# Optimization experiments

Hardware: AMD Instinct MI355X
Metric: run time of the kernel (lower is better)

The kernel has to match this reference:

```python
import jax, jax.numpy as jnp
import numpy as np

HD = 64          # head_dim
PX = 32          # patches_x
PY = 32          # patches_y
IW = 512.0       # image_width
IH = 512.0       # image_height
C = 4            # cameras
B = 1
H = 12
S = C * PX * PY  # 4096


def _rope_coeffs(pos, feat_dim):
    nf = feat_dim // 2
    freqs = 100.0 ** (-jnp.arange(nf, dtype=jnp.float32) / nf)  # freq_base=100, freq_scale=1
    ang = pos[:, None].astype(jnp.float32) * freqs[None, :]
    # broadcast shape (1, seqlen, 1, nf)
    return jnp.cos(ang)[None, :, None, :], jnp.sin(ang)[None, :, None, :]


def _rope(x, cs, inverse=False):
    cos, sin = cs
    h = x.shape[-1] // 2
    xi, yi = x[..., :h], x[..., h:]
    if inverse:
        return jnp.concatenate([cos * xi - sin * yi, sin * xi + cos * yi], -1)
    return jnp.concatenate([cos * xi + sin * yi, -sin * xi + cos * yi], -1)


def _proj(x, M):
    # x: (b, s, n, f), M: (b, c, D, D) per-camera projection applied to D-sized sub-blocks
    b, s, n, f = x.shape
    c, D = M.shape[1], M.shape[-1]
    xr = x.reshape(b, c, s // c, n, f // D, D)
    return jnp.einsum('bcij,bcpnkj->bcpnki', M, xr).reshape(b, s, n, f)


def _invert_SE3(T):
    Rinv = jnp.swapaxes(T[..., :3, :3], -1, -2)
    t = -jnp.einsum('...ij,...j->...i', Rinv, T[..., :3, 3])
    top = jnp.concatenate([Rinv, t[..., None]], -1)            # (..., 3, 4)
    bot = jnp.zeros_like(top[..., :1, :]).at[..., 0, 3].set(1.0)
    return jnp.concatenate([top, bot], -2)


def _lift_K(K):
    out = jnp.zeros(K.shape[:-2] + (4, 4), K.dtype)
    return out.at[..., :3, :3].set(K).at[..., 3, 3].set(1.0)


def _invert_K(K):
    out = jnp.zeros_like(K)
    out = out.at[..., 0, 0].set(1.0 / K[..., 0, 0]).at[..., 1, 1].set(1.0 / K[..., 1, 1])
    out = out.at[..., 0, 2].set(-K[..., 0, 2] / K[..., 0, 0]).at[..., 1, 2].set(-K[..., 1, 2] / K[..., 1, 1])
    return out.at[..., 2, 2].set(1.0)


def setup_inputs() -> dict:
    key = jax.random.key(0)
    kq, kk, kv, kr, kt, kf = jax.random.split(key, 6)
    q = jax.random.normal(kq, (B, S, H, HD), dtype=jnp.float32)
    k = jax.random.normal(kk, (B, S, H, HD), dtype=jnp.float32)
    v = jax.random.normal(kv, (B, S, H, HD), dtype=jnp.float32)
    # proper SE(3) viewmats: random rotations (det +1) + translations
    A = jax.random.normal(kr, (B, C, 3, 3), dtype=jnp.float32)
    Q, _ = jnp.linalg.qr(A)
    Q = Q * jnp.sign(jnp.linalg.det(Q))[..., None, None]  # det(sQ)=s^3 det(Q) for 3x3
    t = jax.random.normal(kt, (B, C, 3, 1), dtype=jnp.float32)
    top = jnp.concatenate([Q, t], -1)
    bot = jnp.tile(jnp.array([0.0, 0.0, 0.0, 1.0], jnp.float32)[None, None, None, :], (B, C, 1, 1))
    viewmats = jnp.concatenate([top, bot], -2)
    # realistic pinhole intrinsics
    f = 400.0 + 200.0 * jax.random.uniform(kf, (B, C, 2), dtype=jnp.float32)
    Ks = jnp.zeros((B, C, 3, 3), jnp.float32)
    Ks = Ks.at[..., 0, 0].set(f[..., 0]).at[..., 1, 1].set(f[..., 1])
    Ks = Ks.at[..., 0, 2].set(IW / 2).at[..., 1, 2].set(IH / 2).at[..., 2, 2].set(1.0)
    return {'q': q, 'k': k, 'v': v, 'viewmats': viewmats, 'Ks': Ks}


def reference(q, k, v, viewmats, Ks):
    # normalize intrinsics to [-0.5, 0.5] image coords
    Ksn = jnp.zeros_like(Ks)
    Ksn = Ksn.at[..., 0, 0].set(Ks[..., 0, 0] / IW).at[..., 1, 1].set(Ks[..., 1, 1] / IH)
    Ksn = Ksn.at[..., 0, 2].set(Ks[..., 0, 2] / IW - 0.5).at[..., 1, 2].set(Ks[..., 1, 2] / IH - 0.5)
    Ksn = Ksn.at[..., 2, 2].set(1.0)
    P = jnp.einsum('...ij,...jk->...ik', _lift_K(Ksn), viewmats)         # (B,C,4,4)
    P_T = jnp.swapaxes(P, -1, -2)
    P_inv = jnp.einsum('...ij,...jk->...ik', _invert_SE3(viewmats), _lift_K(_invert_K(Ksn)))
    # 2-D patch positions, tiled over cameras (num_register_tokens=0)
    pos_x = jnp.tile(jnp.arange(PX), (PY * C,))
    pos_y = jnp.tile(jnp.repeat(jnp.arange(PY), PX), (C,))
    cx = _rope_coeffs(pos_x, HD // 4)
    cy = _rope_coeffs(pos_y, HD // 4)
    h2, h4 = HD // 2, HD // 4

    def tq(x):
        return jnp.concatenate([_proj(x[..., :h2], P_T), _rope(x[..., h2:h2 + h4], cx), _rope(x[..., h2 + h4:], cy)], -1)

    def tkv(x):
        return jnp.concatenate([_proj(x[..., :h2], P_inv), _rope(x[..., h2:h2 + h4], cx), _rope(x[..., h2 + h4:], cy)], -1)

    def to(x):
        return jnp.concatenate([_proj(x[..., :h2], P), _rope(x[..., h2:h2 + h4], cx, True), _rope(x[..., h2 + h4:], cy, True)], -1)

    qh, kh, vh = tq(q), tkv(k), tkv(v)
    scale = 1.0 / jnp.sqrt(jnp.float32(HD))
    scores = jnp.einsum('bqhd,bkhd->bhqk', qh, kh) * scale
    w = jax.nn.softmax(scores, axis=-1)
    out = jnp.einsum('bhqk,bkhd->bqhd', w, vh)
    return to(out)
```

## Files before the change

kernel.cpp:

```cpp
#include <hip/hip_runtime.h>
#include <cstdint>

#define SQ 4096
#define NH 12
#define NC 4
#define KVB 64
#define NSPLIT 2
#define NTS (SQ / NSPLIT / KVB)

typedef __attribute__((ext_vector_type(8))) __bf16 bf16x8;
typedef __attribute__((ext_vector_type(8))) short short8;
typedef __attribute__((ext_vector_type(4))) short s16x4;
typedef __attribute__((ext_vector_type(4))) float f32x4;
typedef __attribute__((ext_vector_type(16))) float f32x16;
typedef __attribute__((ext_vector_type(4))) unsigned int u32x4;
typedef __attribute__((ext_vector_type(2))) unsigned int u32x2;

__device__ __forceinline__ unsigned short f2bf(float f) {
  unsigned int u = __float_as_uint(f);
  u += 0x7FFFu + ((u >> 16) & 1u);
  return (unsigned short)(u >> 16);
}
__device__ __forceinline__ float bf2f(unsigned short u) {
  return __uint_as_float(((unsigned int)u) << 16);
}
__device__ __forceinline__ unsigned int cvtpk(float lo, float hi) {
  unsigned int r;
  asm("v_cvt_pk_bf16_f32 %0, %1, %2" : "=v"(r) : "v"(lo), "v"(hi));
  return r;
}

__device__ __constant__ float FRQ[8] = {
    1.0f, 0.5623413251903491f, 0.31622776601683794f, 0.17782794100389229f,
    0.1f, 0.05623413251903491f, 0.031622776601683794f, 0.017782794100389229f};

__device__ __forceinline__ float4 mat4(const float4 M[4], float4 x) {
  float4 y;
  y.x = M[0].x * x.x + M[0].y * x.y + M[0].z * x.z + M[0].w * x.w;
  y.y = M[1].x * x.x + M[1].y * x.y + M[1].z * x.z + M[1].w * x.w;
  y.z = M[2].x * x.x + M[2].y * x.y + M[2].z * x.z + M[2].w * x.w;
  y.w = M[3].x * x.x + M[3].y * x.y + M[3].z * x.z + M[3].w * x.w;
  return y;
}
__device__ __forceinline__ float4 rope4(float4 x, float4 p, float4 c, float4 sn, float sgn) {
  float4 y;
  y.x = c.x * x.x + sgn * sn.x * p.x;
  y.y = c.y * x.y + sgn * sn.y * p.y;
  y.z = c.z * x.z + sgn * sn.z * p.z;
  y.w = c.w * x.w + sgn * sn.w * p.w;
  return y;
}
__device__ __forceinline__ float4 sxor2(float4 x) {
  float4 p;
  p.x = __shfl_xor(x.x, 2); p.y = __shfl_xor(x.y, 2);
  p.z = __shfl_xor(x.z, 2); p.w = __shfl_xor(x.w, 2);
  return p;
}
__device__ __forceinline__ void store_bf4(unsigned short* p, float4 v) {
  s16x4 r;
  r[0] = (short)f2bf(v.x); r[1] = (short)f2bf(v.y);
  r[2] = (short)f2bf(v.z); r[3] = (short)f2bf(v.w);
  *(s16x4*)p = r;
}

__device__ __forceinline__ void build_tables(const float* __restrict__ viewmats,
                                             const float* __restrict__ Ks,
                                             float* __restrict__ mats,
                                             float* __restrict__ ct, float* __restrict__ st) {
  const int t = threadIdx.x;
  if (t < 256) {
    int pos = t >> 3, jf = t & 7;
    float rev = (float)pos * FRQ[jf] * 0.15915494309189535f;
    ct[t] = __builtin_amdgcn_cosf(rev);
    st[t] = __builtin_amdgcn_sinf(rev);
  }
  if (t < NC) {
    const float* V = viewmats + t * 16;
    const float* K = Ks + t * 9;
    float fx = K[0] * (1.0f / 512.0f);
    float fy = K[4] * (1.0f / 512.0f);
    float cx = K[2] * (1.0f / 512.0f) - 0.5f;
    float cy = K[5] * (1.0f / 512.0f) - 0.5f;
    float P[16], PT[16], IV[16], PI[16];
    for (int jj = 0; jj < 4; jj++) {
      P[0 * 4 + jj] = fx * V[0 * 4 + jj] + cx * V[2 * 4 + jj];
      P[1 * 4 + jj] = fy * V[1 * 4 + jj] + cy * V[2 * 4 + jj];
      P[2 * 4 + jj] = V[2 * 4 + jj];
      P[3 * 4 + jj] = V[3 * 4 + jj];
    }
    for (int i = 0; i < 4; i++)
      for (int jj = 0; jj < 4; jj++) PT[i * 4 + jj] = P[jj * 4 + i];
    for (int i = 0; i < 3; i++) {
      for (int jj = 0; jj < 3; jj++) IV[i * 4 + jj] = V[jj * 4 + i];
      IV[i * 4 + 3] = -(V[3] * V[0 * 4 + i] + V[7] * V[1 * 4 + i] + V[11] * V[2 * 4 + i]);
    }
    IV[12] = 0.f; IV[13] = 0.f; IV[14] = 0.f; IV[15] = 1.f;
    float rfx = 1.0f / fx, rfy = 1.0f / fy;
    for (int i = 0; i < 4; i++) {
      PI[i * 4 + 0] = IV[i * 4 + 0] * rfx;
      PI[i * 4 + 1] = IV[i * 4 + 1] * rfy;
      PI[i * 4 + 2] = -cx * rfx * IV[i * 4 + 0] - cy * rfy * IV[i * 4 + 1] + IV[i * 4 + 2];
      PI[i * 4 + 3] = IV[i * 4 + 3];
    }
    for (int ii = 0; ii < 16; ii++) {
      mats[0   + t * 16 + ii] = PT[ii];
      mats[64  + t * 16 + ii] = PI[ii];
      mats[128 + t * 16 + ii] = P[ii];
    }
  }
}

__global__ __launch_bounds__(256) void transform_kernel(
    const float* __restrict__ q, const float* __restrict__ k, const float* __restrict__ v,
    const float* __restrict__ viewmats, const float* __restrict__ Ks,
    unsigned short* __restrict__ qh, unsigned short* __restrict__ kh, unsigned short* __restrict__ vh) {
  __shared__ float TB[192 + 512];
  float* mats = TB;
  float* CT = TB + 192;
  float* ST = TB + 448;
  build_tables(viewmats, Ks, mats, CT, ST);
  __syncthreads();

  const int t = threadIdx.x;
  const int j = t & 15;
  const int rbase = blockIdx.x * 48;
  const int cam = (rbase / NH) >> 10;

  float4 Mq[4], Mk[4];
  if (j < 8) {
    const float4* mq = (const float4*)(mats + cam * 16);
    const float4* mk = (const float4*)(mats + 64 + cam * 16);
#pragma unroll
    for (int i = 0; i < 4; ++i) { Mq[i] = mq[i]; Mk[i] = mk[i]; }
  }

#pragma unroll
  for (int itr = 0; itr < 3; ++itr) {
    const int row = rbase + itr * 16 + (t >> 4);
    const int s = row / NH;
    const int h = row - s * NH;
    const size_t ioff = (size_t)row * 64 + j * 4;
    const size_t ooff = (size_t)h * (SQ * 64) + (size_t)s * 64 + j * 4;
    float4 xq = *(const float4*)(q + ioff);
    float4 xk = *(const float4*)(k + ioff);
    float4 xv = *(const float4*)(v + ioff);
    float4 pq = sxor2(xq), pk = sxor2(xk), pv = sxor2(xv);
    float4 yq, yk, yv;
    if (j < 8) {
      yq = mat4(Mq, xq); yk = mat4(Mk, xk); yv = mat4(Mk, xv);
    } else {
      bool isx = (((j >> 1) & 1) == 0);
      float sgn = isx ? 1.0f : -1.0f;
      int pos = (j < 12) ? (s & 31) : ((s >> 5) & 31);
      int fb = (j & 1) * 4;
      float4 c = *(const float4*)(CT + pos * 8 + fb);
      float4 sn = *(const float4*)(ST + pos * 8 + fb);
      yq = rope4(xq, pq, c, sn, sgn);
      yk = rope4(xk, pk, c, sn, sgn);
      yv = rope4(xv, pv, c, sn, sgn);
    }
    const float SC = 0.1803368801111204f;
    yq.x *= SC; yq.y *= SC; yq.z *= SC; yq.w *= SC;
    store_bf4(qh + ooff, yq);
    store_bf4(kh + ooff, yk);
    store_bf4(vh + ooff, yv);
  }
}

__global__ __launch_bounds__(128, 3) void attn_kernel(const unsigned short* __restrict__ qh,
                                                      const unsigned short* __restrict__ kh,
                                                      const unsigned short* __restrict__ vh,
                                                      unsigned short* __restrict__ opart,
                                                      float* __restrict__ lbuf) {
  __shared__ __align__(16) short Kl[2][KVB * 64];
  __shared__ __align__(16) short Vl[2][KVB * 64];
  const int t = threadIdx.x;
  const int lane = t & 63;
  const int w = t >> 6;
  const int hi = lane >> 5;
  const int l31 = lane & 31;
  const int sw7 = l31 & 7;
  const int h = blockIdx.y;
  const int sp = blockIdx.z;
  const int q0 = blockIdx.x * 64 + w * 32;
  const int kbase = sp * (SQ / NSPLIT);
  const size_t hbase = (size_t)h * SQ * 64;

  bf16x8 qf[4];
  {
    const unsigned short* qp = qh + hbase + (size_t)(q0 + l31) * 64 + hi * 8;
#pragma unroll
    for (int ds = 0; ds < 4; ++ds) qf[ds] = *(const bf16x8*)(qp + ds * 16);
  }

  int kr[4], kg[4], kidx[4];
#pragma unroll
  for (int i = 0; i < 4; ++i) {
    int c = t + 128 * i;
    kr[i] = c >> 3;
    kg[i] = c & 7;
    kidx[i] = kr[i] * 64 + ((kg[i] ^ (kr[i] & 7)) << 3);
  }
  const int va = t & 15;
  const int vD0 = (t >> 4) * 8;

  float l = 0.f;
  f32x16 oac0, oac1;
#pragma unroll
  for (int r = 0; r < 16; ++r) { oac0[r] = 0.f; oac1[r] = 0.f; }

  short8 kst[4], vst[4];

  auto issue_loads = [&](int kt) {
#pragma unroll
    for (int i = 0; i < 4; ++i)
      kst[i] = *(const short8*)(kh + hbase + (size_t)(kt + kr[i]) * 64 + kg[i] * 8);
    const unsigned short* vp = vh + hbase + (size_t)(kt + 4 * va) * 64 + vD0;
#pragma unroll
    for (int i = 0; i < 4; ++i) vst[i] = *(const short8*)(vp + i * 64);
  };

  auto write_lds = [&](int buf) {
    short* K = Kl[buf];
#pragma unroll
    for (int i = 0; i < 4; ++i) *(short8*)(K + kidx[i]) = kst[i];
    short* V = Vl[buf];
#pragma unroll
    for (int dd = 0; dd < 8; ++dd) {
      int d = vD0 + dd;
      unsigned int w0 = (unsigned int)(unsigned short)vst[0][dd] |
                        ((unsigned int)(unsigned short)vst[1][dd] << 16);
      unsigned int w1 = (unsigned int)(unsigned short)vst[2][dd] |
                        ((unsigned int)(unsigned short)vst[3][dd] << 16);
      u32x2 pk; pk[0] = w0; pk[1] = w1;
      int idx = d * 64 + ((((va >> 1)) ^ (d & 7)) << 3) + (va & 1) * 4;
      *(u32x2*)(V + idx) = pk;
    }
  };

  issue_loads(kbase);
  write_lds(0);
  __syncthreads();

#define MKFRAG(sv, base, out)                                          \
  {                                                                    \
    unsigned int a0 = cvtpk(sv[base + 0], sv[base + 1]);               \
    unsigned int b0 = cvtpk(sv[base + 4], sv[base + 5]);               \
    asm volatile("v_permlane32_swap_b32 %0, %1" : "+v"(a0), "+v"(b0)); \
    unsigned int a1 = cvtpk(sv[base + 2], sv[base + 3]);               \
    unsigned int b1 = cvtpk(sv[base + 6], sv[base + 7]);               \
    asm volatile("v_permlane32_swap_b32 %0, %1" : "+v"(a1), "+v"(b1)); \
    u32x4 u; u[0] = a0; u[1] = a1; u[2] = b0; u[3] = b1;               \
    out = __builtin_bit_cast(bf16x8, u);                               \
  }

  for (int it = 0; it < NTS; ++it) {
    const int cur = it & 1;
    const bool pf = (it + 1 < NTS);
    if (pf) issue_loads(kbase + (it + 1) * KVB);

    const short* K = Kl[cur];
    const short* V = Vl[cur];

    f32x16 s0, s1;
#pragma unroll
    for (int r = 0; r < 16; ++r) { s0[r] = 0.f; s1[r] = 0.f; }
    __builtin_amdgcn_s_setprio(1);
#pragma unroll
    for (int ds = 0; ds < 4; ++ds) {
      bf16x8 k0 = *(const bf16x8*)(K + (0 * 32 + l31) * 64 + (((hi + 2 * ds) ^ sw7) << 3));
      bf16x8 k1 = *(const bf16x8*)(K + (1 * 32 + l31) * 64 + (((hi + 2 * ds) ^ sw7) << 3));
      s0 = __builtin_amdgcn_mfma_f32_32x32x16_bf16(k0, qf[ds], s0, 0, 0, 0);
      s1 = __builtin_amdgcn_mfma_f32_32x32x16_bf16(k1, qf[ds], s1, 0, 0, 0);
    }
    __builtin_amdgcn_s_setprio(0);

    float rs = 0.f;
#pragma unroll
    for (int r = 0; r < 16; ++r) { s0[r] = __builtin_amdgcn_exp2f(s0[r]); rs += s0[r]; }
#pragma unroll
    for (int r = 0; r < 16; ++r) { s1[r] = __builtin_amdgcn_exp2f(s1[r]); rs += s1[r]; }
    rs += __shfl_xor(rs, 32);
    l += rs;

    bf16x8 pa00, pa01, pa10, pa11;
    MKFRAG(s0, 0, pa00);
    MKFRAG(s0, 8, pa01);
    MKFRAG(s1, 0, pa10);
    MKFRAG(s1, 8, pa11);

    __builtin_amdgcn_s_setprio(1);
#pragma unroll
    for (int db = 0; db < 2; ++db) {
      const int rb = (db * 32 + l31) * 64;
      bf16x8 v00 = *(const bf16x8*)(V + rb + (((0 + hi) ^ sw7) << 3));
      bf16x8 v01 = *(const bf16x8*)(V + rb + (((2 + hi) ^ sw7) << 3));
      bf16x8 v10 = *(const bf16x8*)(V + rb + (((4 + hi) ^ sw7) << 3));
      bf16x8 v11 = *(const bf16x8*)(V + rb + (((6 + hi) ^ sw7) << 3));
      if (db == 0) {
        oac0 = __builtin_amdgcn_mfma_f32_32x32x16_bf16(pa00, v00, oac0, 0, 0, 0);
        oac0 = __builtin_amdgcn_mfma_f32_32x32x16_bf16(pa01, v01, oac0, 0, 0, 0);
        oac0 = __builtin_amdgcn_mfma_f32_32x32x16_bf16(pa10, v10, oac0, 0, 0, 0);
        oac0 = __builtin_amdgcn_mfma_f32_32x32x16_bf16(pa11, v11, oac0, 0, 0, 0);
      } else {
        oac1 = __builtin_amdgcn_mfma_f32_32x32x16_bf16(pa00, v00, oac1, 0, 0, 0);
        oac1 = __builtin_amdgcn_mfma_f32_32x32x16_bf16(pa01, v01, oac1, 0, 0, 0);
        oac1 = __builtin_amdgcn_mfma_f32_32x32x16_bf16(pa10, v10, oac1, 0, 0, 0);
        oac1 = __builtin_amdgcn_mfma_f32_32x32x16_bf16(pa11, v11, oac1, 0, 0, 0);
      }
    }
    __builtin_amdgcn_s_setprio(0);

    if (pf) {
      write_lds(cur ^ 1);
      __syncthreads();
    }
  }

  float linv = 1.0f / l;
  unsigned short* op = opart + (size_t)sp * NH * SQ * 64 + hbase;
#pragma unroll
  for (int r = 0; r < 16; ++r) {
    int qrow = (r & 3) + 8 * (r >> 2) + 4 * hi;
    float lv = __shfl(linv, qrow);
    op[(size_t)(q0 + qrow) * 64 + l31] = f2bf(oac0[r] * lv);
    op[(size_t)(q0 + qrow) * 64 + 32 + l31] = f2bf(oac1[r] * lv);
  }
  if (hi == 0) lbuf[(size_t)sp * NH * SQ + (size_t)h * SQ + q0 + l31] = l;
}

__global__ __launch_bounds__(256) void outtr_kernel(const unsigned short* __restrict__ opart,
                                                    const float* __restrict__ lbuf,
                                                    const float* __restrict__ viewmats,
                                                    const float* __restrict__ Ks,
                                                    float* __restrict__ out) {
  __shared__ float TB[192 + 512];
  float* mats = TB;
  float* CT = TB + 192;
  float* ST = TB + 448;
  build_tables(viewmats, Ks, mats, CT, ST);
  __syncthreads();

  const int t = threadIdx.x;
  const int j = t & 15;
  const int rbase = blockIdx.x * 48;
  const int cam = (rbase / NH) >> 10;

  float4 M[4];
  if (j < 8) {
    const float4* mp = (const float4*)(mats + 128 + cam * 16);
#pragma unroll
    for (int i = 0; i < 4; ++i) M[i] = mp[i];
  }

#pragma unroll
  for (int itr = 0; itr < 3; ++itr) {
    const int row = rbase + itr * 16 + (t >> 4);
    const int s = row / NH;
    const int h = row - s * NH;

    float l1 = lbuf[(size_t)h * SQ + s];
    float l2 = lbuf[(size_t)NH * SQ + (size_t)h * SQ + s];
    float inv = 1.0f / (l1 + l2);
    float w1 = l1 * inv, w2 = l2 * inv;

    const size_t po = (size_t)h * (SQ * 64) + (size_t)s * 64 + j * 4;
    s16x4 r1 = *(const s16x4*)(opart + po);
    s16x4 r2 = *(const s16x4*)(opart + (size_t)NH * SQ * 64 + po);
    float4 x;
    x.x = bf2f((unsigned short)r1[0]) * w1 + bf2f((unsigned short)r2[0]) * w2;
    x.y = bf2f((unsigned short)r1[1]) * w1 + bf2f((unsigned short)r2[1]) * w2;
    x.z = bf2f((unsigned short)r1[2]) * w1 + bf2f((unsigned short)r2[2]) * w2;
    x.w = bf2f((unsigned short)r1[3]) * w1 + bf2f((unsigned short)r2[3]) * w2;

    float4 p = sxor2(x);
    float4 y;
    if (j < 8) {
      y = mat4(M, x);
    } else {
      bool isx = (((j >> 1) & 1) == 0);
      float sgn = isx ? -1.0f : 1.0f;
      int pos = (j < 12) ? (s & 31) : ((s >> 5) & 31);
      int fb = (j & 1) * 4;
      float4 c = *(const float4*)(CT + pos * 8 + fb);
      float4 sn = *(const float4*)(ST + pos * 8 + fb);
      y = rope4(x, p, c, sn, sgn);
    }
    *(float4*)(out + (size_t)row * 64 + j * 4) = y;
  }
}

extern "C" void kernel_launch(void* const* d_in, const int* in_sizes, int n_in,
                              void* d_out, int out_size, void* d_ws, size_t ws_size,
                              hipStream_t stream) {
  const float* q = (const float*)d_in[0];
  const float* k = (const float*)d_in[1];
  const float* v = (const float*)d_in[2];
  const float* vm = (const float*)d_in[3];
  const float* Ks = (const float*)d_in[4];

  char* ws = (char*)d_ws;
  const size_t HSZ = (size_t)NH * SQ * 64;
  unsigned short* qh = (unsigned short*)(ws + 4096);
  unsigned short* kh = qh + HSZ;
  unsigned short* vh = kh + HSZ;
  unsigned short* opart = vh + HSZ;
  float* lbuf = (float*)(opart + (size_t)NSPLIT * HSZ);

  hipLaunchKernelGGL(transform_kernel, dim3((SQ * NH) / 48), dim3(256), 0, stream,
                     q, k, v, vm, Ks, qh, kh, vh);
  hipLaunchKernelGGL(attn_kernel, dim3(SQ / 64, NH, NSPLIT), dim3(128), 0, stream,
                     qh, kh, vh, opart, lbuf);
  hipLaunchKernelGGL(outtr_kernel, dim3((SQ * NH) / 48), dim3(256), 0, stream,
                     opart, lbuf, vm, Ks, (float*)d_out);
}
```

Before: 193.1 us.

## Split KV range four ways and single-buffer LDS tiles in attention

Raises the KV split count from two to four, so the attention grid launches twice as many blocks, each covering half as many KV tiles. The combine kernel is generalized to merge any number of partials. The LDS double buffer is reduced to a single buffer with an extra barrier before each refill, halving shared memory per block to allow more resident blocks. In exchange it adds an extra sync per iteration and doubles partial-output traffic in the combine pass.

```diff
diff --git a/kernel.cpp b/kernel.cpp
--- a/kernel.cpp
+++ b/kernel.cpp
@@ -5,7 +5,7 @@
 #define NH 12
 #define NC 4
 #define KVB 64
-#define NSPLIT 2
+#define NSPLIT 4
 #define NTS (SQ / NSPLIT / KVB)
 
 typedef __attribute__((ext_vector_type(8))) __bf16 bf16x8;
@@ -172,8 +172,8 @@
                                                       const unsigned short* __restrict__ vh,
                                                       unsigned short* __restrict__ opart,
                                                       float* __restrict__ lbuf) {
-  __shared__ __align__(16) short Kl[2][KVB * 64];
-  __shared__ __align__(16) short Vl[2][KVB * 64];
+  __shared__ __align__(16) short Kl[KVB * 64];
+  __shared__ __align__(16) short Vl[KVB * 64];
   const int t = threadIdx.x;
   const int lane = t & 63;
   const int w = t >> 6;
@@ -220,11 +220,9 @@
     for (int i = 0; i < 4; ++i) vst[i] = *(const short8*)(vp + i * 64);
   };
 
-  auto write_lds = [&](int buf) {
-    short* K = Kl[buf];
-#pragma unroll
-    for (int i = 0; i < 4; ++i) *(short8*)(K + kidx[i]) = kst[i];
-    short* V = Vl[buf];
+  auto write_lds = [&]() {
+#pragma unroll
+    for (int i = 0; i < 4; ++i) *(short8*)(Kl + kidx[i]) = kst[i];
 #pragma unroll
     for (int dd = 0; dd < 8; ++dd) {
       int d = vD0 + dd;
@@ -234,12 +232,12 @@
                         ((unsigned int)(unsigned short)vst[3][dd] << 16);
       u32x2 pk; pk[0] = w0; pk[1] = w1;
       int idx = d * 64 + ((((va >> 1)) ^ (d & 7)) << 3) + (va & 1) * 4;
-      *(u32x2*)(V + idx) = pk;
+      *(u32x2*)(Vl + idx) = pk;
     }
   };
 
   issue_loads(kbase);
-  write_lds(0);
+  write_lds();
   __syncthreads();
 
 #define MKFRAG(sv, base, out)                                          \
@@ -255,21 +253,17 @@
   }
 
   for (int it = 0; it < NTS; ++it) {
-    const int cur = it & 1;
     const bool pf = (it + 1 < NTS);
     if (pf) issue_loads(kbase + (it + 1) * KVB);
 
-    const short* K = Kl[cur];
-    const short* V = Vl[cur];
-
     f32x16 s0, s1;
 #pragma unroll
     for (int r = 0; r < 16; ++r) { s0[r] = 0.f; s1[r] = 0.f; }
     __builtin_amdgcn_s_setprio(1);
 #pragma unroll
     for (int ds = 0; ds < 4; ++ds) {
-      bf16x8 k0 = *(const bf16x8*)(K + (0 * 32 + l31) * 64 + (((hi + 2 * ds) ^ sw7) << 3));
-      bf16x8 k1 = *(const bf16x8*)(K + (1 * 32 + l31) * 64 + (((hi + 2 * ds) ^ sw7) << 3));
+      bf16x8 k0 = *(const bf16x8*)(Kl + (0 * 32 + l31) * 64 + (((hi + 2 * ds) ^ sw7) << 3));
+      bf16x8 k1 = *(const bf16x8*)(Kl + (1 * 32 + l31) * 64 + (((hi + 2 * ds) ^ sw7) << 3));
       s0 = __builtin_amdgcn_mfma_f32_32x32x16_bf16(k0, qf[ds], s0, 0, 0, 0);
       s1 = __builtin_amdgcn_mfma_f32_32x32x16_bf16(k1, qf[ds], s1, 0, 0, 0);
     }
@@ -293,10 +287,10 @@
 #pragma unroll
     for (int db = 0; db < 2; ++db) {
       const int rb = (db * 32 + l31) * 64;
-      bf16x8 v00 = *(const bf16x8*)(V + rb + (((0 + hi) ^ sw7) << 3));
-      bf16x8 v01 = *(const bf16x8*)(V + rb + (((2 + hi) ^ sw7) << 3));
-      bf16x8 v10 = *(const bf16x8*)(V + rb + (((4 + hi) ^ sw7) << 3));
-      bf16x8 v11 = *(const bf16x8*)(V + rb + (((6 + hi) ^ sw7) << 3));
+      bf16x8 v00 = *(const bf16x8*)(Vl + rb + (((0 + hi) ^ sw7) << 3));
+      bf16x8 v01 = *(const bf16x8*)(Vl + rb + (((2 + hi) ^ sw7) << 3));
+      bf16x8 v10 = *(const bf16x8*)(Vl + rb + (((4 + hi) ^ sw7) << 3));
+      bf16x8 v11 = *(const bf16x8*)(Vl + rb + (((6 + hi) ^ sw7) << 3));
       if (db == 0) {
         oac0 = __builtin_amdgcn_mfma_f32_32x32x16_bf16(pa00, v00, oac0, 0, 0, 0);
         oac0 = __builtin_amdgcn_mfma_f32_32x32x16_bf16(pa01, v01, oac0, 0, 0, 0);
@@ -310,9 +304,9 @@
       }
     }
     __builtin_amdgcn_s_setprio(0);
-
+    __syncthreads();
     if (pf) {
-      write_lds(cur ^ 1);
+      write_lds();
       __syncthreads();
     }
   }
@@ -359,19 +353,27 @@
     const int s = row / NH;
     const int h = row - s * NH;
 
-    float l1 = lbuf[(size_t)h * SQ + s];
-    float l2 = lbuf[(size_t)NH * SQ + (size_t)h * SQ + s];
-    float inv = 1.0f / (l1 + l2);
-    float w1 = l1 * inv, w2 = l2 * inv;
+    const size_t HSZ = (size_t)NH * SQ * 64;
+    float lv[NSPLIT];
+    float lsum = 0.f;
+#pragma unroll
+    for (int sp = 0; sp < NSPLIT; ++sp) {
+      lv[sp] = lbuf[(size_t)sp * NH * SQ + (size_t)h * SQ + s];
+      lsum += lv[sp];
+    }
+    float inv = 1.0f / lsum;
 
     const size_t po = (size_t)h * (SQ * 64) + (size_t)s * 64 + j * 4;
-    s16x4 r1 = *(const s16x4*)(opart + po);
-    s16x4 r2 = *(const s16x4*)(opart + (size_t)NH * SQ * 64 + po);
-    float4 x;
-    x.x = bf2f((unsigned short)r1[0]) * w1 + bf2f((unsigned short)r2[0]) * w2;
-    x.y = bf2f((unsigned short)r1[1]) * w1 + bf2f((unsigned short)r2[1]) * w2;
-    x.z = bf2f((unsigned short)r1[2]) * w1 + bf2f((unsigned short)r2[2]) * w2;
-    x.w = bf2f((unsigned short)r1[3]) * w1 + bf2f((unsigned short)r2[3]) * w2;
+    float4 x = make_float4(0.f, 0.f, 0.f, 0.f);
+#pragma unroll
+    for (int sp = 0; sp < NSPLIT; ++sp) {
+      s16x4 rr = *(const s16x4*)(opart + (size_t)sp * HSZ + po);
+      float wv = lv[sp] * inv;
+      x.x += bf2f((unsigned short)rr[0]) * wv;
+      x.y += bf2f((unsigned short)rr[1]) * wv;
+      x.z += bf2f((unsigned short)rr[2]) * wv;
+      x.w += bf2f((unsigned short)rr[3]) * wv;
+    }
 
     float4 p = sxor2(x);
     float4 y;
```

Measured after the change: 178.0 us. 7.8% less time.
